# Kernel tuning notes

Measured on AMD Instinct MI355X. Metric: run time of the kernel, lower is better.

Reference implementation:

```python
import jax, jax.numpy as jnp
import numpy as np
import math

B = 2048
INPUT_SIZE = 1024
OUTPUT_SIZE = 512
SPONGE = 1024
ACT = 256
REC = 256
STORE = ACT + REC  # 512
DEPTH = 8
BDEPTH = 10
NEUTRAL_C = 1.0
SQRT2 = math.sqrt(2.0)


def _make_structure():
    # Deterministic stand-in for the module's random.sample-based recall wiring.
    rng = np.random.RandomState(0)
    half = (SPONGE + 1) // 2
    shuffle_perm = np.array([i // 2 + (i % 2) * half for i in range(SPONGE)], dtype=np.int64)
    unused = []
    recall = []
    for i in range(DEPTH):
        unused.extend(range(i * STORE, (i + 1) * STORE))
        sel = rng.choice(len(unused), size=REC, replace=False)
        sel_set = set(sel.tolist())
        recall.append([unused[k] for k in sorted(sel_set)])
        unused = [u for k, u in enumerate(unused) if k not in sel_set]
    out_mem = np.array(sorted(unused), dtype=np.int64)  # 2048 leftover memory columns
    bf_size = len(out_mem) + SPONGE  # 3072
    bf_depth = int(math.ceil(math.log2(bf_size)))  # 12
    bf_half = (bf_size + 1) // 2
    bf_perm = np.array([i // 2 + (i % 2) * bf_half for i in range(bf_size)], dtype=np.int64)
    return shuffle_perm, np.array(recall, dtype=np.int64), out_mem, bf_perm, bf_size, bf_depth


def setup_inputs() -> dict:
    key = jax.random.key(0)
    ks = jax.random.split(key, 6)
    shuffle_perm, recall_idx, out_mem_idx, bf_perm, bf_size, bf_depth = _make_structure()
    return {
        "X": jax.random.normal(ks[0], (B, INPUT_SIZE), jnp.float32),
        "scales": jnp.ones((INPUT_SIZE,), jnp.float32),
        "angles": jax.random.uniform(ks[1], (DEPTH, BDEPTH, SPONGE // 2), jnp.float32) * (2 * math.pi),
        "act_bias": jax.random.normal(ks[2], (DEPTH, ACT), jnp.float32),
        "act_activation": jax.random.normal(ks[3], (DEPTH, ACT), jnp.float32),
        "act_curvature": jax.random.normal(ks[4], (DEPTH, ACT), jnp.float32),
        "bf_angles": jax.random.uniform(ks[5], (bf_depth, bf_size // 2), jnp.float32) * (2 * math.pi),
        "shuffle_perm": jnp.asarray(shuffle_perm),
        "recall_idx": jnp.asarray(recall_idx),
        "output_mem_idx": jnp.asarray(out_mem_idx),
        "bf_perm": jnp.asarray(bf_perm),
    }


def _base_activation(x, c):
    # In the source, `a` is overwritten with torch.tensor(1.0), so a == 1.
    t = (math.pi / 4) / c
    y0 = (1.0 / c) * (1.0 / SQRT2 - math.cos(math.pi / 2))  # = 1/(c*sqrt(2))
    m0 = math.sin(math.pi / 2)  # = 1
    y1 = (1.0 / c) * (1.0 / SQRT2 - 1.0)
    m1 = math.sin(0.0)  # = 0
    mid = (1.0 / c) * (1.0 / SQRT2 - jnp.cos(math.pi / 4 + c * x))
    return jnp.where(x > t, y0 + m0 * (x - t), jnp.where(x < -t, y1 + m1 * (x + t), mid))


def _butterfly(x, angles, perm):
    # angles: [n_layers, exch]; shuffle -> Givens rotation per pair, extra passthrough
    exch = angles.shape[1]
    for j in range(angles.shape[0]):
        s = x[:, perm]
        x1, x2 = s[:, :exch], s[:, exch:2 * exch]
        ca, sa = jnp.cos(angles[j]), jnp.sin(angles[j])
        x = jnp.concatenate([ca * x1 + sa * x2, -sa * x1 + ca * x2, s[:, 2 * exch:]], axis=1)
    return x


def reference(X, scales, angles, act_bias, act_activation, act_curvature, bf_angles,
              shuffle_perm, recall_idx, output_mem_idx, bf_perm):
    Xs = X * scales
    sponge = Xs[:, :SPONGE]  # input_size == sponge_size: no zero pad, memory[0] is empty
    mem = jnp.zeros((Xs.shape[0], DEPTH * STORE), Xs.dtype)
    for i in range(DEPTH):
        sponge = _butterfly(sponge, angles[i], shuffle_perm)
        x1 = sponge[:, STORE:STORE + ACT] + act_bias[i]  # activation_position == store_size
        c = 0.5 * NEUTRAL_C * (act_curvature[i] + jnp.sqrt(act_curvature[i] ** 2 + 1.0))
        ap = _base_activation(x1, c)
        am = _base_activation(-x1, c)
        act_out = jnp.stack([ap, am], axis=2).reshape(ap.shape[0], 2 * ACT)  # interleave +/-
        mem = mem.at[:, i * STORE:(i + 1) * STORE].set(sponge[:, :STORE])
        recall = mem[:, recall_idx[i]]  # indices only address already-filled columns
        # [act_out | sponge[store:act_pos] (empty) | sponge[act_pos+ACT:] | recall]
        sponge = jnp.concatenate([act_out, sponge[:, STORE + ACT:], recall], axis=1)
    pre = jnp.concatenate([mem[:, output_mem_idx], sponge], axis=1)  # [B, 3072]
    out = _butterfly(pre, bf_angles, bf_perm)
    return out[:, :OUTPUT_SIZE]
```

## Files before the change

### kernel.cpp

```cpp
#include <hip/hip_runtime.h>
#include <math.h>

#define NB 2048
#define DEPTH 8

#define FTAB_OFF    0
#define BF01_OFF    81920
#define BFF_OFF     88064
#define ACT4_OFF    98304
#define PHYSA_OFF   106496
#define PHYSR_OFF   110592
#define PHYSO2_OFF  112640

#define MB0 4608
#define EXB 4608

#define WFENCE() asm volatile("s_waitcnt lgkmcnt(0)" ::: "memory")

__global__ void setup_kernel(const float* __restrict__ angles,
                             const float* __restrict__ bf_angles,
                             const float* __restrict__ act_bias,
                             const float* __restrict__ act_curv,
                             const int* __restrict__ recall_idx,
                             const int* __restrict__ out_mem_idx,
                             float* __restrict__ ws) {
    __shared__ int physL[4096];
    if (blockIdx.x < 200) {
        int id = blockIdx.x * 256 + threadIdx.x;
        if (id < 40960) {
            int w = id & 3, t = (id >> 2) & 255, dg = id >> 10;
            int d = dg / 5, g = dg - 5 * d;
            int a = 2 * (t & 127) + (t >> 7);
            int pair = (w == 0) ? a : (w == 1) ? (a + 256)
                     : (w == 2) ? (2 * a) : (2 * a + 1);
            int st = 2 * g + (w >> 1);
            float ang = angles[(d * 10 + st) * 512 + pair];
            float s, c; __sincosf(ang, &s, &c);
            ws[FTAB_OFF + 2 * id]     = c;
            ws[FTAB_OFF + 2 * id + 1] = s;
        } else if (id < 44032) {
            int e = id - 40960;
            int w = e & 3; int ti = e >> 2;
            int t = ti / 3; int i = ti - 3 * t;
            int a = t + 256 * i;
            int pair = (w == 0) ? a : (w == 1) ? (a + 768)
                     : (w == 2) ? (2 * a) : (2 * a + 1);
            int stage = (w < 2) ? 0 : 1;
            float ang = bf_angles[stage * 1536 + pair];
            float s, c; __sincosf(ang, &s, &c);
            ws[BF01_OFF + 2 * e]     = c;
            ws[BF01_OFF + 2 * e + 1] = s;
        } else if (id < 49152) {
            int e = id - 44032;
            int f = e >> 10; int rem = e & 1023; int t = rem >> 2; int w = rem & 3;
            int P;
            if (f == 0) P = 3 * t;
            else if (f < 4) { int k = 8 - 2 * f;
                              P = ((t >> (2 * f)) * (768 >> k)) + (t & ((256 >> k) - 1)); }
            else P = t;
            int pair = (w == 0) ? P : (w == 1) ? (P + 768)
                     : (w == 2) ? (2 * P) : (2 * P + 1);
            int stage = (w < 2) ? (2 + 2 * f) : (3 + 2 * f);
            float ang = bf_angles[stage * 1536 + pair];
            float s, c; __sincosf(ang, &s, &c);
            ws[BFF_OFF + 2 * e]     = c;
            ws[BFF_OFF + 2 * e + 1] = s;
        } else if (id < 51200) {
            int ida = id - 49152;
            float cu = act_curv[ida];
            float c  = 0.5f * (cu + sqrtf(cu * cu + 1.0f));
            ((float4*)(ws + ACT4_OFF))[ida] =
                make_float4(act_bias[ida], c, 1.0f / c, 0.0f);
        }
    } else {
        int tid = threadIdx.x;
        for (int e = tid; e < 4096; e += 256) {
            int v = e, p;
            for (;;) {
                int d = v >> 9, j = v & 511;
                if (d == 0)  { p = j; break; }
                if (j < 256) { p = 256 + d * 256 + j; break; }
                v = recall_idx[(d - 1) * 256 + (j - 256)];
            }
            physL[e] = p;
        }
        __syncthreads();
        int* pa = (int*)(ws + PHYSA_OFF);
        for (int e = tid; e < 2048; e += 256) {
            int d = e >> 8, t = e & 255;
            int a = 2 * (t & 127) + (t >> 7);
            pa[2 * e]     = 2 * physL[d * 512 + 2 * a];
            pa[2 * e + 1] = 2 * physL[d * 512 + 2 * a + 1];
        }
        int* pr = (int*)(ws + PHYSR_OFF);
        for (int e = tid; e < 2048; e += 256)
            pr[e] = 2 * physL[recall_idx[e]];
        int* po = (int*)(ws + PHYSO2_OFF);
        for (int e = tid; e < 3072; e += 256) {
            int tt = e / 12; int r = e - 12 * tt; int i = r >> 2; int k = r & 3;
            int a = tt + 256 * i;
            int tl2 = a >> 1, th2 = a & 1;
            int pos = tl2 + 1536 * th2 + 384 * k;
            po[e] = (pos < 2048) ? 2 * physL[out_mem_idx[pos]]
                                 : MB0 + 2 * (pos - 2048);
        }
    }
}

__device__ __forceinline__ float actf(float x, float c, float ic) {
    const float is2 = 0.70710678118654752f;
    float tt = 0.78539816339744831f * ic;
    float y0 = is2 * ic;
    float y1 = (is2 - 1.0f) * ic;
    float mid = ic * (is2 - __cosf(0.78539816339744831f + c * x));
    return x > tt ? (y0 + (x - tt)) : (x < -tt ? y1 : mid);
}

__launch_bounds__(64, 2)
__global__ void sponge_kernel(const float* __restrict__ X,
                              const float* __restrict__ scales,
                              const float* __restrict__ ws,
                              float* __restrict__ out) {
    __shared__ float L[6656];
    const int lane = threadIdx.x;
    const int rowA = blockIdx.x * 2;

    const float4* ftab   = (const float4*)(ws + FTAB_OFF);
    const float4* bf01   = (const float4*)(ws + BF01_OFF);
    const float4* bff    = (const float4*)(ws + BFF_OFF);
    const float4* act4   = (const float4*)(ws + ACT4_OFF);
    const int2*   physA  = (const int2*)(ws + PHYSA_OFF);
    const int*    physr  = (const int*)(ws + PHYSR_OFF);
    const int*    physo2 = (const int*)(ws + PHYSO2_OFF);

    float hA[4][4], hB[4][4];
    {
        const float* Xr0 = X + (size_t)rowA * 1024;
        const float* Xr1 = Xr0 + 1024;
#pragma unroll
        for (int q = 0; q < 4; ++q) {
            int tq = lane + 64 * q;
            int b  = (tq & 127) + (tq >> 7) * 512;
#pragma unroll
            for (int k = 0; k < 4; ++k) {
                float s = scales[b + 128 * k];
                hA[q][k] = Xr0[b + 128 * k] * s;
                hB[q][k] = Xr1[b + 128 * k] * s;
            }
        }
    }

#define DQUAD(cA, cB, i0, i1, i2, i3, F0, F1, F2, F3)                    \
    { float g0 =  (cA).x * (i0) + (cA).y * (i2);                         \
      float g2 = -(cA).y * (i0) + (cA).x * (i2);                         \
      float g1 =  (cA).z * (i1) + (cA).w * (i3);                         \
      float g3 = -(cA).w * (i1) + (cA).z * (i3);                         \
      F0 =  (cB).x * g0 + (cB).y * g1;                                   \
      F2 = -(cB).y * g0 + (cB).x * g1;                                   \
      F1 =  (cB).z * g2 + (cB).w * g3;                                   \
      F3 = -(cB).w * g2 + (cB).z * g3; }

    float4 cs[4][2];
    int fb = 0;
#define LOADC()                                                          \
    { _Pragma("unroll")                                                  \
      for (int q = 0; q < 4; ++q) {                                      \
          int tq = lane + 64 * q;                                        \
          cs[q][0] = ftab[fb + 2 * tq];                                  \
          cs[q][1] = ftab[fb + 2 * tq + 1];                              \
      } fb += 512; }

    LOADC();

#pragma unroll 1
    for (int d = 0; d < DEPTH; ++d) {
        float4 av[2][4]; int pr2[2][2]; int2 pmv[4];
#pragma unroll
        for (int q = 0; q < 2; ++q) {
            int k0 = (lane + 64 * q) >> 1;
#pragma unroll
            for (int j = 0; j < 4; ++j) av[q][j] = act4[d * 256 + k0 + 64 * j];
            int u = lane + 64 * q;
            pr2[q][0] = physr[d * 256 + u];
            pr2[q][1] = physr[d * 256 + u + 128];
        }
#pragma unroll
        for (int q = 0; q < 4; ++q) pmv[q] = physA[d * 256 + lane + 64 * q];

        for (int g = 0; g < 4; ++g) {
#pragma unroll
            for (int q = 0; q < 4; ++q) {
                int tq = lane + 64 * q;
                int tl = tq & 127, th = tq >> 7;
                int WI = 2 * (2 * (tl & 15) + 32 * th + 64 * (tl >> 4));
                float fA0, fA1, fA2, fA3, fB0, fB1, fB2, fB3;
                DQUAD(cs[q][0], cs[q][1], hA[q][0], hA[q][1], hA[q][2], hA[q][3],
                      fA0, fA1, fA2, fA3);
                DQUAD(cs[q][0], cs[q][1], hB[q][0], hB[q][1], hB[q][2], hB[q][3],
                      fB0, fB1, fB2, fB3);
                *(float4*)(L + EXB + WI)        = make_float4(fA0, fB0, fA1, fB1);
                *(float4*)(L + EXB + WI + 1024) = make_float4(fA2, fB2, fA3, fB3);
            }
            WFENCE();
            LOADC();
#pragma unroll
            for (int q = 0; q < 4; ++q) {
                int tq = lane + 64 * q;
                int tl = tq & 127, th = tq >> 7;
                int RI = 2 * ((tl & 1) + 2 * ((tl >> 2) & 15) + 32 * ((tl >> 1) & 1)
                             + 64 * (tl >> 6) + 512 * th);
                float2 e0 = *(const float2*)(L + EXB + RI);
                float2 e1 = *(const float2*)(L + EXB + RI + 256);
                float2 e2 = *(const float2*)(L + EXB + RI + 512);
                float2 e3 = *(const float2*)(L + EXB + RI + 768);
                hA[q][0] = e0.x; hB[q][0] = e0.y; hA[q][1] = e1.x; hB[q][1] = e1.y;
                hA[q][2] = e2.x; hB[q][2] = e2.y; hA[q][3] = e3.x; hB[q][3] = e3.y;
            }
            WFENCE();
        }

#pragma unroll
        for (int q = 0; q < 4; ++q) {
            int tq = lane + 64 * q;
            int tl = tq & 127, th = tq >> 7;
            int aq = 2 * tl + th;
            float fA0, fA1, fA2, fA3, fB0, fB1, fB2, fB3;
            DQUAD(cs[q][0], cs[q][1], hA[q][0], hA[q][1], hA[q][2], hA[q][3],
                  fA0, fA1, fA2, fA3);
            DQUAD(cs[q][0], cs[q][1], hB[q][0], hB[q][1], hB[q][2], hB[q][3],
                  fB0, fB1, fB2, fB3);
            *(float2*)(L + pmv[q].x) = make_float2(fA0, fB0);
            *(float2*)(L + pmv[q].y) = make_float2(fA1, fB1);
            *(float4*)(L + EXB + 4 * aq) = make_float4(fA2, fB2, fA3, fB3);
        }
        WFENCE();
        if (d < DEPTH - 1) LOADC();
        {
            const float* Z = L + EXB;
#pragma unroll
            for (int q = 0; q < 2; ++q) {
                int tq = lane + 64 * q;
                int k0 = tq >> 1;
                float sgn = (tq & 1) ? -1.0f : 1.0f;
                float2 z0 = *(const float2*)(Z + 2 * k0);
                float2 z1 = *(const float2*)(Z + 2 * k0 + 128);
                float2 z2 = *(const float2*)(Z + 2 * k0 + 256);
                float2 z3 = *(const float2*)(Z + 2 * k0 + 384);
                hA[q][0] = actf(sgn * (z0.x + av[q][0].x), av[q][0].y, av[q][0].z);
                hB[q][0] = actf(sgn * (z0.y + av[q][0].x), av[q][0].y, av[q][0].z);
                hA[q][1] = actf(sgn * (z1.x + av[q][1].x), av[q][1].y, av[q][1].z);
                hB[q][1] = actf(sgn * (z1.y + av[q][1].x), av[q][1].y, av[q][1].z);
                hA[q][2] = actf(sgn * (z2.x + av[q][2].x), av[q][2].y, av[q][2].z);
                hB[q][2] = actf(sgn * (z2.y + av[q][2].x), av[q][2].y, av[q][2].z);
                hA[q][3] = actf(sgn * (z3.x + av[q][3].x), av[q][3].y, av[q][3].z);
                hB[q][3] = actf(sgn * (z3.y + av[q][3].x), av[q][3].y, av[q][3].z);
            }
#pragma unroll
            for (int q = 0; q < 2; ++q) {
                int u = lane + 64 * q;
                float2 k0v = *(const float2*)(Z + 512 + 2 * u);
                float2 k1v = *(const float2*)(Z + 768 + 2 * u);
                float2 rc0 = *(const float2*)(L + pr2[q][0]);
                float2 rc1 = *(const float2*)(L + pr2[q][1]);
                hA[2 + q][0] = k0v.x; hB[2 + q][0] = k0v.y;
                hA[2 + q][1] = k1v.x; hB[2 + q][1] = k1v.y;
                hA[2 + q][2] = rc0.x; hB[2 + q][2] = rc0.y;
                hA[2 + q][3] = rc1.x; hB[2 + q][3] = rc1.y;
            }
        }
        WFENCE();
    }

    int4 pga[4][3];
#pragma unroll
    for (int q = 0; q < 4; ++q) {
        const int4* pgp = (const int4*)(physo2 + (lane + 64 * q) * 12);
#pragma unroll
        for (int j = 0; j < 3; ++j) pga[q][j] = pgp[j];
    }
#pragma unroll
    for (int q = 0; q < 4; ++q) {
        int tq = lane + 64 * q;
        int b  = (tq & 127) + (tq >> 7) * 512;
        *(float2*)(L + EXB + 2 * b)       = make_float2(hA[q][0], hB[q][0]);
        *(float2*)(L + EXB + 2 * b + 256) = make_float2(hA[q][1], hB[q][1]);
        *(float2*)(L + EXB + 2 * b + 512) = make_float2(hA[q][2], hB[q][2]);
        *(float2*)(L + EXB + 2 * b + 768) = make_float2(hA[q][3], hB[q][3]);
    }
    WFENCE();

    float2 w[4][12];
#pragma unroll
    for (int q = 0; q < 4; ++q) {
        int4 pg = pga[q][0];
        w[q][0] = *(const float2*)(L + pg.x); w[q][1] = *(const float2*)(L + pg.y);
        w[q][2] = *(const float2*)(L + pg.z); w[q][3] = *(const float2*)(L + pg.w);
        pg = pga[q][1];
        w[q][4] = *(const float2*)(L + pg.x); w[q][5] = *(const float2*)(L + pg.y);
        w[q][6] = *(const float2*)(L + pg.z); w[q][7] = *(const float2*)(L + pg.w);
        pg = pga[q][2];
        w[q][8]  = *(const float2*)(L + pg.x); w[q][9]  = *(const float2*)(L + pg.y);
        w[q][10] = *(const float2*)(L + pg.z); w[q][11] = *(const float2*)(L + pg.w);
    }
    WFENCE();

#pragma unroll
    for (int q = 0; q < 4; ++q) {
        int tq = lane + 64 * q;
#pragma unroll
        for (int i = 0; i < 3; ++i) {
            float4 c01 = bf01[(tq * 3 + i) * 2];
            float4 c23 = bf01[(tq * 3 + i) * 2 + 1];
            float yA0, yA1, yA2, yA3, yB0, yB1, yB2, yB3;
            DQUAD(c01, c23, w[q][4*i].x, w[q][4*i+1].x, w[q][4*i+2].x, w[q][4*i+3].x,
                  yA0, yA1, yA2, yA3);
            DQUAD(c01, c23, w[q][4*i].y, w[q][4*i+1].y, w[q][4*i+2].y, w[q][4*i+3].y,
                  yB0, yB1, yB2, yB3);
            *(float4*)(L + 4 * tq + 1024 * i)        = make_float4(yA0, yB0, yA1, yB1);
            *(float4*)(L + 4 * tq + 1024 * i + 3072) = make_float4(yA2, yB2, yA3, yB3);
        }
    }
    WFENCE();

#pragma unroll
    for (int f = 0; f < 4; ++f) {
        float2 x1p[4], x1r[4], x2p[4], x2r[4];
        float4 cS[4], cT[4];
        int Pq[4];
#pragma unroll
        for (int q = 0; q < 4; ++q) {
            int tq = lane + 64 * q;
            cS[q] = bff[(f * 256 + tq) * 2];
            cT[q] = bff[(f * 256 + tq) * 2 + 1];
            int P;
            if (f == 0) P = 3 * tq;
            else { const int k = 8 - 2 * f;
                   P = ((tq >> (2 * f)) * (768 >> k)) + (tq & ((256 >> k) - 1)); }
            Pq[q] = P;
            int base = 2 * ((P >> 1) + (P & 1) * 1536);
            x1p[q] = *(const float2*)(L + base);
            x1r[q] = *(const float2*)(L + base + 768);
            x2p[q] = *(const float2*)(L + base + 1536);
            x2r[q] = *(const float2*)(L + base + 2304);
        }
        WFENCE();
#pragma unroll
        for (int q = 0; q < 4; ++q) {
            float4 csS = cS[q], csT = cT[q];
            float o1P =  csS.x * x1p[q].x + csS.y * x2p[q].x;
            float o2P = -csS.y * x1p[q].x + csS.x * x2p[q].x;
            float o1Q =  csS.z * x1r[q].x + csS.w * x2r[q].x;
            float o2Q = -csS.w * x1r[q].x + csS.z * x2r[q].x;
            float yA0 =  csT.x * o1P + csT.y * o1Q;
            float yA2 = -csT.y * o1P + csT.x * o1Q;
            float yA1 =  csT.z * o2P + csT.w * o2Q;
            float yA3 = -csT.w * o2P + csT.z * o2Q;
            o1P =  csS.x * x1p[q].y + csS.y * x2p[q].y;
            o2P = -csS.y * x1p[q].y + csS.x * x2p[q].y;
            o1Q =  csS.z * x1r[q].y + csS.w * x2r[q].y;
            o2Q = -csS.w * x1r[q].y + csS.z * x2r[q].y;
            float yB0 =  csT.x * o1P + csT.y * o1Q;
            float yB2 = -csT.y * o1P + csT.x * o1Q;
            float yB1 =  csT.z * o2P + csT.w * o2Q;
            float yB3 = -csT.w * o2P + csT.z * o2Q;
            *(float4*)(L + 4 * Pq[q])        = make_float4(yA0, yB0, yA1, yB1);
            *(float4*)(L + 4 * Pq[q] + 3072) = make_float4(yA2, yB2, yA3, yB3);
        }
        WFENCE();
    }

#pragma unroll
    for (int q = 0; q < 4; ++q) {
        int tq = lane + 64 * q;
        int base = 2 * ((tq >> 1) + (tq & 1) * 1536);
        float4 csS = bff[(4 * 256 + tq) * 2];
        float4 csT = bff[(4 * 256 + tq) * 2 + 1];
        float2 x1p = *(const float2*)(L + base);
        float2 x1r = *(const float2*)(L + base + 768);
        float2 x2p = *(const float2*)(L + base + 1536);
        float2 x2r = *(const float2*)(L + base + 2304);
        float o1P =  csS.x * x1p.x + csS.y * x2p.x;
        float o2P = -csS.y * x1p.x + csS.x * x2p.x;
        float o1Q =  csS.z * x1r.x + csS.w * x2r.x;
        float o2Q = -csS.w * x1r.x + csS.z * x2r.x;
        *(float2*)(out + (size_t)rowA * 512 + 2 * tq) =
            make_float2(csT.x * o1P + csT.y * o1Q, csT.z * o2P + csT.w * o2Q);
        o1P =  csS.x * x1p.y + csS.y * x2p.y;
        o2P = -csS.y * x1p.y + csS.x * x2p.y;
        o1Q =  csS.z * x1r.y + csS.w * x2r.y;
        o2Q = -csS.w * x1r.y + csS.z * x2r.y;
        *(float2*)(out + (size_t)(rowA + 1) * 512 + 2 * tq) =
            make_float2(csT.x * o1P + csT.y * o1Q, csT.z * o2P + csT.w * o2Q);
    }
#undef DQUAD
#undef LOADC
}

extern "C" void kernel_launch(void* const* d_in, const int* in_sizes, int n_in,
                              void* d_out, int out_size, void* d_ws, size_t ws_size,
                              hipStream_t stream) {
    const float* X          = (const float*)d_in[0];
    const float* scales     = (const float*)d_in[1];
    const float* angles     = (const float*)d_in[2];
    const float* act_bias   = (const float*)d_in[3];
    const float* act_curv   = (const float*)d_in[5];
    const float* bf_angles  = (const float*)d_in[6];
    const int*   recall_idx  = (const int*)d_in[8];
    const int*   out_mem_idx = (const int*)d_in[9];

    float* ws = (float*)d_ws;

    setup_kernel<<<201, 256, 0, stream>>>(angles, bf_angles, act_bias, act_curv,
                                          recall_idx, out_mem_idx, ws);
    sponge_kernel<<<NB / 2, 64, 0, stream>>>(X, scales, ws, (float*)d_out);
}
```

Before: 134.1 us.

## Process one row per wave with four waves per block instead of two rows per wave

Each block now runs four 64-lane waves, and each wave handles a single row in its own LDS slice, where before one wave handled two interleaved rows. This halves the register state per lane and allows higher occupancy, trading away the shared reuse of twiddle coefficients across two rows. The explicit lgkmcnt fences are removed and relied on wave-local ordering instead. The setup kernel now resolves the recall chain level by level in LDS rather than by pointer-chasing through global memory.

Measured after the change: 123.1 us. 8.2% less time.

```diff
diff --git a/kernel.cpp b/kernel.cpp
--- a/kernel.cpp
+++ b/kernel.cpp
@@ -12,10 +12,8 @@
 #define PHYSR_OFF   110592
 #define PHYSO2_OFF  112640
 
-#define MB0 4608
-#define EXB 4608
-
-#define WFENCE() asm volatile("s_waitcnt lgkmcnt(0)" ::: "memory")
+#define EXB 2304
+#define RSZ 3328
 
 __global__ void setup_kernel(const float* __restrict__ angles,
                              const float* __restrict__ bf_angles,
@@ -25,6 +23,8 @@
                              const int* __restrict__ out_mem_idx,
                              float* __restrict__ ws) {
     __shared__ int physL[4096];
+    __shared__ int rcl[2048];
+    __shared__ int oml[2048];
     if (blockIdx.x < 200) {
         int id = blockIdx.x * 256 + threadIdx.x;
         if (id < 40960) {
@@ -74,35 +74,37 @@
         }
     } else {
         int tid = threadIdx.x;
-        for (int e = tid; e < 4096; e += 256) {
-            int v = e, p;
-            for (;;) {
-                int d = v >> 9, j = v & 511;
-                if (d == 0)  { p = j; break; }
-                if (j < 256) { p = 256 + d * 256 + j; break; }
-                v = recall_idx[(d - 1) * 256 + (j - 256)];
-            }
-            physL[e] = p;
-        }
+        for (int e = tid; e < 2048; e += 256) rcl[e] = recall_idx[e];
+        for (int e = tid; e < 2048; e += 256) oml[e] = out_mem_idx[e];
+        for (int e = tid; e < 512; e += 256) physL[e] = e;
         __syncthreads();
+        for (int d = 1; d < 8; ++d) {
+            for (int j = tid; j < 512; j += 256) {
+                int p;
+                if (j < 256) p = 256 + d * 256 + j;
+                else          p = physL[rcl[(d - 1) * 256 + (j - 256)]];
+                physL[512 * d + j] = p;
+            }
+            __syncthreads();
+        }
         int* pa = (int*)(ws + PHYSA_OFF);
         for (int e = tid; e < 2048; e += 256) {
             int d = e >> 8, t = e & 255;
             int a = 2 * (t & 127) + (t >> 7);
-            pa[2 * e]     = 2 * physL[d * 512 + 2 * a];
-            pa[2 * e + 1] = 2 * physL[d * 512 + 2 * a + 1];
+            pa[2 * e]     = physL[d * 512 + 2 * a];
+            pa[2 * e + 1] = physL[d * 512 + 2 * a + 1];
         }
         int* pr = (int*)(ws + PHYSR_OFF);
         for (int e = tid; e < 2048; e += 256)
-            pr[e] = 2 * physL[recall_idx[e]];
+            pr[e] = physL[rcl[e]];
         int* po = (int*)(ws + PHYSO2_OFF);
         for (int e = tid; e < 3072; e += 256) {
             int tt = e / 12; int r = e - 12 * tt; int i = r >> 2; int k = r & 3;
             int a = tt + 256 * i;
             int tl2 = a >> 1, th2 = a & 1;
             int pos = tl2 + 1536 * th2 + 384 * k;
-            po[e] = (pos < 2048) ? 2 * physL[out_mem_idx[pos]]
-                                 : MB0 + 2 * (pos - 2048);
+            po[e] = (pos < 2048) ? physL[oml[pos]]
+                                 : EXB + (pos - 2048);
         }
     }
 }
@@ -116,38 +118,44 @@
     return x > tt ? (y0 + (x - tt)) : (x < -tt ? y1 : mid);
 }
 
-__launch_bounds__(64, 2)
+__launch_bounds__(256, 3)
 __global__ void sponge_kernel(const float* __restrict__ X,
                               const float* __restrict__ scales,
                               const float* __restrict__ ws,
                               float* __restrict__ out) {
-    __shared__ float L[6656];
-    const int lane = threadIdx.x;
-    const int rowA = blockIdx.x * 2;
-
-    const float4* ftab   = (const float4*)(ws + FTAB_OFF);
-    const float4* bf01   = (const float4*)(ws + BF01_OFF);
-    const float4* bff    = (const float4*)(ws + BFF_OFF);
-    const float4* act4   = (const float4*)(ws + ACT4_OFF);
-    const int2*   physA  = (const int2*)(ws + PHYSA_OFF);
-    const int*    physr  = (const int*)(ws + PHYSR_OFF);
-    const int*    physo2 = (const int*)(ws + PHYSO2_OFF);
-
-    float hA[4][4], hB[4][4];
+    __shared__ float Lall[4 * RSZ];
+    const int lane = threadIdx.x & 63;
+    const int wvid = threadIdx.x >> 6;
+    float* __restrict__ L = Lall + wvid * RSZ;
+    const int row = blockIdx.x * 4 + wvid;
+
+    const float4* bf01  = (const float4*)(ws + BF01_OFF);
+    const float4* bff   = (const float4*)(ws + BFF_OFF);
+    const float4* act4  = (const float4*)(ws + ACT4_OFF);
+    const int2* physA  = (const int2*)(ws + PHYSA_OFF);
+    const int*  physr  = (const int*)(ws + PHYSR_OFF);
+    const int*  physo2 = (const int*)(ws + PHYSO2_OFF);
+
+    int Wn[4], Rn[4], Bq[4], Aq[4];
+#pragma unroll
+    for (int q = 0; q < 4; ++q) {
+        int tq = lane + 64 * q;
+        int tl = tq & 127, th = tq >> 7;
+        Wn[q] = 2 * (tl & 15) + 32 * th + 64 * (tl >> 4);
+        Rn[q] = (tl & 1) + 2 * ((tl >> 2) & 15) + 32 * ((tl >> 1) & 1)
+              + 64 * (tl >> 6) + 512 * th;
+        Bq[q] = tl + th * 512;
+        Aq[q] = 2 * tl + th;
+    }
+
+    float h[4][4];
     {
-        const float* Xr0 = X + (size_t)rowA * 1024;
-        const float* Xr1 = Xr0 + 1024;
-#pragma unroll
-        for (int q = 0; q < 4; ++q) {
-            int tq = lane + 64 * q;
-            int b  = (tq & 127) + (tq >> 7) * 512;
-#pragma unroll
-            for (int k = 0; k < 4; ++k) {
-                float s = scales[b + 128 * k];
-                hA[q][k] = Xr0[b + 128 * k] * s;
-                hB[q][k] = Xr1[b + 128 * k] * s;
-            }
-        }
+        const float* Xr = X + (size_t)row * 1024;
+#pragma unroll
+        for (int q = 0; q < 4; ++q)
+#pragma unroll
+            for (int k = 0; k < 4; ++k)
+                h[q][k] = Xr[Bq[q] + 128 * k] * scales[Bq[q] + 128 * k];
     }
 
 #define DQUAD(cA, cB, i0, i1, i2, i3, F0, F1, F2, F3)                    \
@@ -158,18 +166,18 @@
       F0 =  (cB).x * g0 + (cB).y * g1;                                   \
       F2 = -(cB).y * g0 + (cB).x * g1;                                   \
       F1 =  (cB).z * g2 + (cB).w * g3;                                   \
-      F3 = -(cB).w * g2 + (cB).z * g3; }
-
-    float4 cs[4][2];
+      F3 =  -(cB).w * g2 + (cB).z * g3; }
+
+    const float4* ftab = (const float4*)(ws + FTAB_OFF);
     int fb = 0;
+    float4 csA[4], csB[4];
 #define LOADC()                                                          \
     { _Pragma("unroll")                                                  \
       for (int q = 0; q < 4; ++q) {                                      \
           int tq = lane + 64 * q;                                        \
-          cs[q][0] = ftab[fb + 2 * tq];                                  \
-          cs[q][1] = ftab[fb + 2 * tq + 1];                              \
+          csA[q] = ftab[fb + 2 * tq];                                    \
+          csB[q] = ftab[fb + 2 * tq + 1];                                \
       } fb += 512; }
-
     LOADC();
 
 #pragma unroll 1
@@ -177,98 +185,70 @@
         float4 av[2][4]; int pr2[2][2]; int2 pmv[4];
 #pragma unroll
         for (int q = 0; q < 2; ++q) {
-            int k0 = (lane + 64 * q) >> 1;
+            int tq = lane + 64 * q;
+            int k0 = tq >> 1;
 #pragma unroll
             for (int j = 0; j < 4; ++j) av[q][j] = act4[d * 256 + k0 + 64 * j];
-            int u = lane + 64 * q;
-            pr2[q][0] = physr[d * 256 + u];
-            pr2[q][1] = physr[d * 256 + u + 128];
+            pr2[q][0] = physr[d * 256 + tq];
+            pr2[q][1] = physr[d * 256 + tq + 128];
         }
 #pragma unroll
         for (int q = 0; q < 4; ++q) pmv[q] = physA[d * 256 + lane + 64 * q];
 
+#pragma unroll
         for (int g = 0; g < 4; ++g) {
+            float f[4][4];
+#pragma unroll
+            for (int q = 0; q < 4; ++q)
+                DQUAD(csA[q], csB[q], h[q][0], h[q][1], h[q][2], h[q][3],
+                      f[q][0], f[q][1], f[q][2], f[q][3]);
 #pragma unroll
             for (int q = 0; q < 4; ++q) {
-                int tq = lane + 64 * q;
-                int tl = tq & 127, th = tq >> 7;
-                int WI = 2 * (2 * (tl & 15) + 32 * th + 64 * (tl >> 4));
-                float fA0, fA1, fA2, fA3, fB0, fB1, fB2, fB3;
-                DQUAD(cs[q][0], cs[q][1], hA[q][0], hA[q][1], hA[q][2], hA[q][3],
-                      fA0, fA1, fA2, fA3);
-                DQUAD(cs[q][0], cs[q][1], hB[q][0], hB[q][1], hB[q][2], hB[q][3],
-                      fB0, fB1, fB2, fB3);
-                *(float4*)(L + EXB + WI)        = make_float4(fA0, fB0, fA1, fB1);
-                *(float4*)(L + EXB + WI + 1024) = make_float4(fA2, fB2, fA3, fB3);
-            }
-            WFENCE();
+                *(float2*)(L + EXB + Wn[q])       = make_float2(f[q][0], f[q][1]);
+                *(float2*)(L + EXB + Wn[q] + 512) = make_float2(f[q][2], f[q][3]);
+            }
             LOADC();
 #pragma unroll
             for (int q = 0; q < 4; ++q) {
-                int tq = lane + 64 * q;
-                int tl = tq & 127, th = tq >> 7;
-                int RI = 2 * ((tl & 1) + 2 * ((tl >> 2) & 15) + 32 * ((tl >> 1) & 1)
-                             + 64 * (tl >> 6) + 512 * th);
-                float2 e0 = *(const float2*)(L + EXB + RI);
-                float2 e1 = *(const float2*)(L + EXB + RI + 256);
-                float2 e2 = *(const float2*)(L + EXB + RI + 512);
-                float2 e3 = *(const float2*)(L + EXB + RI + 768);
-                hA[q][0] = e0.x; hB[q][0] = e0.y; hA[q][1] = e1.x; hB[q][1] = e1.y;
-                hA[q][2] = e2.x; hB[q][2] = e2.y; hA[q][3] = e3.x; hB[q][3] = e3.y;
-            }
-            WFENCE();
-        }
-
-#pragma unroll
-        for (int q = 0; q < 4; ++q) {
-            int tq = lane + 64 * q;
-            int tl = tq & 127, th = tq >> 7;
-            int aq = 2 * tl + th;
-            float fA0, fA1, fA2, fA3, fB0, fB1, fB2, fB3;
-            DQUAD(cs[q][0], cs[q][1], hA[q][0], hA[q][1], hA[q][2], hA[q][3],
-                  fA0, fA1, fA2, fA3);
-            DQUAD(cs[q][0], cs[q][1], hB[q][0], hB[q][1], hB[q][2], hB[q][3],
-                  fB0, fB1, fB2, fB3);
-            *(float2*)(L + pmv[q].x) = make_float2(fA0, fB0);
-            *(float2*)(L + pmv[q].y) = make_float2(fA1, fB1);
-            *(float4*)(L + EXB + 4 * aq) = make_float4(fA2, fB2, fA3, fB3);
-        }
-        WFENCE();
-        if (d < DEPTH - 1) LOADC();
+                h[q][0] = L[EXB + Rn[q]];
+                h[q][1] = L[EXB + Rn[q] + 128];
+                h[q][2] = L[EXB + Rn[q] + 256];
+                h[q][3] = L[EXB + Rn[q] + 384];
+            }
+        }
         {
+            float f[4][4];
+#pragma unroll
+            for (int q = 0; q < 4; ++q)
+                DQUAD(csA[q], csB[q], h[q][0], h[q][1], h[q][2], h[q][3],
+                      f[q][0], f[q][1], f[q][2], f[q][3]);
+#pragma unroll
+            for (int q = 0; q < 4; ++q) {
+                L[pmv[q].x] = f[q][0];
+                L[pmv[q].y] = f[q][1];
+                *(float2*)(L + EXB + 2 * Aq[q]) = make_float2(f[q][2], f[q][3]);
+            }
+            if (d < DEPTH - 1) LOADC();
             const float* Z = L + EXB;
 #pragma unroll
             for (int q = 0; q < 2; ++q) {
                 int tq = lane + 64 * q;
                 int k0 = tq >> 1;
                 float sgn = (tq & 1) ? -1.0f : 1.0f;
-                float2 z0 = *(const float2*)(Z + 2 * k0);
-                float2 z1 = *(const float2*)(Z + 2 * k0 + 128);
-                float2 z2 = *(const float2*)(Z + 2 * k0 + 256);
-                float2 z3 = *(const float2*)(Z + 2 * k0 + 384);
-                hA[q][0] = actf(sgn * (z0.x + av[q][0].x), av[q][0].y, av[q][0].z);
-                hB[q][0] = actf(sgn * (z0.y + av[q][0].x), av[q][0].y, av[q][0].z);
-                hA[q][1] = actf(sgn * (z1.x + av[q][1].x), av[q][1].y, av[q][1].z);
-                hB[q][1] = actf(sgn * (z1.y + av[q][1].x), av[q][1].y, av[q][1].z);
-                hA[q][2] = actf(sgn * (z2.x + av[q][2].x), av[q][2].y, av[q][2].z);
-                hB[q][2] = actf(sgn * (z2.y + av[q][2].x), av[q][2].y, av[q][2].z);
-                hA[q][3] = actf(sgn * (z3.x + av[q][3].x), av[q][3].y, av[q][3].z);
-                hB[q][3] = actf(sgn * (z3.y + av[q][3].x), av[q][3].y, av[q][3].z);
+                h[q][0] = actf(sgn * (Z[k0]       + av[q][0].x), av[q][0].y, av[q][0].z);
+                h[q][1] = actf(sgn * (Z[k0 + 64]  + av[q][1].x), av[q][1].y, av[q][1].z);
+                h[q][2] = actf(sgn * (Z[k0 + 128] + av[q][2].x), av[q][2].y, av[q][2].z);
+                h[q][3] = actf(sgn * (Z[k0 + 192] + av[q][3].x), av[q][3].y, av[q][3].z);
             }
 #pragma unroll
             for (int q = 0; q < 2; ++q) {
                 int u = lane + 64 * q;
-                float2 k0v = *(const float2*)(Z + 512 + 2 * u);
-                float2 k1v = *(const float2*)(Z + 768 + 2 * u);
-                float2 rc0 = *(const float2*)(L + pr2[q][0]);
-                float2 rc1 = *(const float2*)(L + pr2[q][1]);
-                hA[2 + q][0] = k0v.x; hB[2 + q][0] = k0v.y;
-                hA[2 + q][1] = k1v.x; hB[2 + q][1] = k1v.y;
-                hA[2 + q][2] = rc0.x; hB[2 + q][2] = rc0.y;
-                hA[2 + q][3] = rc1.x; hB[2 + q][3] = rc1.y;
-            }
-        }
-        WFENCE();
+                h[2 + q][0] = Z[256 + u];
+                h[2 + q][1] = Z[384 + u];
+                h[2 + q][2] = L[pr2[q][0]];
+                h[2 + q][3] = L[pr2[q][1]];
+            }
+        }
     }
 
     int4 pga[4][3];
@@ -280,30 +260,21 @@
     }
 #pragma unroll
     for (int q = 0; q < 4; ++q) {
-        int tq = lane + 64 * q;
-        int b  = (tq & 127) + (tq >> 7) * 512;
-        *(float2*)(L + EXB + 2 * b)       = make_float2(hA[q][0], hB[q][0]);
-        *(float2*)(L + EXB + 2 * b + 256) = make_float2(hA[q][1], hB[q][1]);
-        *(float2*)(L + EXB + 2 * b + 512) = make_float2(hA[q][2], hB[q][2]);
-        *(float2*)(L + EXB + 2 * b + 768) = make_float2(hA[q][3], hB[q][3]);
-    }
-    WFENCE();
-
-    float2 w[4][12];
+        L[EXB + Bq[q]]       = h[q][0];
+        L[EXB + Bq[q] + 128] = h[q][1];
+        L[EXB + Bq[q] + 256] = h[q][2];
+        L[EXB + Bq[q] + 384] = h[q][3];
+    }
+    float w[4][12];
 #pragma unroll
     for (int q = 0; q < 4; ++q) {
         int4 pg = pga[q][0];
-        w[q][0] = *(const float2*)(L + pg.x); w[q][1] = *(const float2*)(L + pg.y);
-        w[q][2] = *(const float2*)(L + pg.z); w[q][3] = *(const float2*)(L + pg.w);
+        w[q][0] = L[pg.x]; w[q][1] = L[pg.y]; w[q][2] = L[pg.z]; w[q][3] = L[pg.w];
         pg = pga[q][1];
-        w[q][4] = *(const float2*)(L + pg.x); w[q][5] = *(const float2*)(L + pg.y);
-        w[q][6] = *(const float2*)(L + pg.z); w[q][7] = *(const float2*)(L + pg.w);
+        w[q][4] = L[pg.x]; w[q][5] = L[pg.y]; w[q][6] = L[pg.z]; w[q][7] = L[pg.w];
         pg = pga[q][2];
-        w[q][8]  = *(const float2*)(L + pg.x); w[q][9]  = *(const float2*)(L + pg.y);
-        w[q][10] = *(const float2*)(L + pg.z); w[q][11] = *(const float2*)(L + pg.w);
-    }
-    WFENCE();
-
+        w[q][8] = L[pg.x]; w[q][9] = L[pg.y]; w[q][10] = L[pg.z]; w[q][11] = L[pg.w];
+    }
 #pragma unroll
     for (int q = 0; q < 4; ++q) {
         int tq = lane + 64 * q;
@@ -311,86 +282,63 @@
         for (int i = 0; i < 3; ++i) {
             float4 c01 = bf01[(tq * 3 + i) * 2];
             float4 c23 = bf01[(tq * 3 + i) * 2 + 1];
-            float yA0, yA1, yA2, yA3, yB0, yB1, yB2, yB3;
-            DQUAD(c01, c23, w[q][4*i].x, w[q][4*i+1].x, w[q][4*i+2].x, w[q][4*i+3].x,
-                  yA0, yA1, yA2, yA3);
-            DQUAD(c01, c23, w[q][4*i].y, w[q][4*i+1].y, w[q][4*i+2].y, w[q][4*i+3].y,
-                  yB0, yB1, yB2, yB3);
-            *(float4*)(L + 4 * tq + 1024 * i)        = make_float4(yA0, yB0, yA1, yB1);
-            *(float4*)(L + 4 * tq + 1024 * i + 3072) = make_float4(yA2, yB2, yA3, yB3);
-        }
-    }
-    WFENCE();
-
+            float y0, y1, y2, y3;
+            DQUAD(c01, c23, w[q][4 * i], w[q][4 * i + 1], w[q][4 * i + 2], w[q][4 * i + 3],
+                  y0, y1, y2, y3);
+            *(float2*)(L + 2 * tq + 512 * i)        = make_float2(y0, y1);
+            *(float2*)(L + 2 * tq + 512 * i + 1536) = make_float2(y2, y3);
+        }
+    }
 #pragma unroll
     for (int f = 0; f < 4; ++f) {
-        float2 x1p[4], x1r[4], x2p[4], x2r[4];
-        float4 cS[4], cT[4];
-        int Pq[4];
+        float x1[4], x2[4], x3[4], x4[4];
+        float4 cS[4], cT[4]; int Pq[4];
 #pragma unroll
         for (int q = 0; q < 4; ++q) {
             int tq = lane + 64 * q;
-            cS[q] = bff[(f * 256 + tq) * 2];
-            cT[q] = bff[(f * 256 + tq) * 2 + 1];
             int P;
             if (f == 0) P = 3 * tq;
             else { const int k = 8 - 2 * f;
                    P = ((tq >> (2 * f)) * (768 >> k)) + (tq & ((256 >> k) - 1)); }
             Pq[q] = P;
-            int base = 2 * ((P >> 1) + (P & 1) * 1536);
-            x1p[q] = *(const float2*)(L + base);
-            x1r[q] = *(const float2*)(L + base + 768);
-            x2p[q] = *(const float2*)(L + base + 1536);
-            x2r[q] = *(const float2*)(L + base + 2304);
-        }
-        WFENCE();
+            int base = (P >> 1) + (P & 1) * 1536;
+            cS[q] = bff[(f * 256 + tq) * 2];
+            cT[q] = bff[(f * 256 + tq) * 2 + 1];
+            x1[q] = L[base];
+            x2[q] = L[base + 384];
+            x3[q] = L[base + 768];
+            x4[q] = L[base + 1152];
+        }
 #pragma unroll
         for (int q = 0; q < 4; ++q) {
-            float4 csS = cS[q], csT = cT[q];
-            float o1P =  csS.x * x1p[q].x + csS.y * x2p[q].x;
-            float o2P = -csS.y * x1p[q].x + csS.x * x2p[q].x;
-            float o1Q =  csS.z * x1r[q].x + csS.w * x2r[q].x;
-            float o2Q = -csS.w * x1r[q].x + csS.z * x2r[q].x;
-            float yA0 =  csT.x * o1P + csT.y * o1Q;
-            float yA2 = -csT.y * o1P + csT.x * o1Q;
-            float yA1 =  csT.z * o2P + csT.w * o2Q;
-            float yA3 = -csT.w * o2P + csT.z * o2Q;
-            o1P =  csS.x * x1p[q].y + csS.y * x2p[q].y;
-            o2P = -csS.y * x1p[q].y + csS.x * x2p[q].y;
-            o1Q =  csS.z * x1r[q].y + csS.w * x2r[q].y;
-            o2Q = -csS.w * x1r[q].y + csS.z * x2r[q].y;
-            float yB0 =  csT.x * o1P + csT.y * o1Q;
-            float yB2 = -csT.y * o1P + csT.x * o1Q;
-            float yB1 =  csT.z * o2P + csT.w * o2Q;
-            float yB3 = -csT.w * o2P + csT.z * o2Q;
-            *(float4*)(L + 4 * Pq[q])        = make_float4(yA0, yB0, yA1, yB1);
-            *(float4*)(L + 4 * Pq[q] + 3072) = make_float4(yA2, yB2, yA3, yB3);
-        }
-        WFENCE();
-    }
-
+            float o1P =  cS[q].x * x1[q] + cS[q].y * x3[q];
+            float o2P = -cS[q].y * x1[q] + cS[q].x * x3[q];
+            float o1Q =  cS[q].z * x2[q] + cS[q].w * x4[q];
+            float o2Q = -cS[q].w * x2[q] + cS[q].z * x4[q];
+            float y0 =  cT[q].x * o1P + cT[q].y * o1Q;
+            float y2 = -cT[q].y * o1P + cT[q].x * o1Q;
+            float y1 =  cT[q].z * o2P + cT[q].w * o2Q;
+            float y3 = -cT[q].w * o2P + cT[q].z * o2Q;
+            *(float2*)(L + 2 * Pq[q])        = make_float2(y0, y1);
+            *(float2*)(L + 2 * Pq[q] + 1536) = make_float2(y2, y3);
+        }
+    }
 #pragma unroll
     for (int q = 0; q < 4; ++q) {
         int tq = lane + 64 * q;
-        int base = 2 * ((tq >> 1) + (tq & 1) * 1536);
-        float4 csS = bff[(4 * 256 + tq) * 2];
-        float4 csT = bff[(4 * 256 + tq) * 2 + 1];
-        float2 x1p = *(const float2*)(L + base);
-        float2 x1r = *(const float2*)(L + base + 768);
-        float2 x2p = *(const float2*)(L + base + 1536);
-        float2 x2r = *(const float2*)(L + base + 2304);
-        float o1P =  csS.x * x1p.x + csS.y * x2p.x;
-        float o2P = -csS.y * x1p.x + csS.x * x2p.x;
-        float o1Q =  csS.z * x1r.x + csS.w * x2r.x;
-        float o2Q = -csS.w * x1r.x + csS.z * x2r.x;
-        *(float2*)(out + (size_t)rowA * 512 + 2 * tq) =
-            make_float2(csT.x * o1P + csT.y * o1Q, csT.z * o2P + csT.w * o2Q);
-        o1P =  csS.x * x1p.y + csS.y * x2p.y;
-        o2P = -csS.y * x1p.y + csS.x * x2p.y;
-        o1Q =  csS.z * x1r.y + csS.w * x2r.y;
-        o2Q = -csS.w * x1r.y + csS.z * x2r.y;
-        *(float2*)(out + (size_t)(rowA + 1) * 512 + 2 * tq) =
-            make_float2(csT.x * o1P + csT.y * o1Q, csT.z * o2P + csT.w * o2Q);
+        int base = (tq >> 1) + (tq & 1) * 1536;
+        float4 cS = bff[(4 * 256 + tq) * 2];
+        float4 cT = bff[(4 * 256 + tq) * 2 + 1];
+        float x1 = L[base];
+        float x2 = L[base + 384];
+        float x3 = L[base + 768];
+        float x4 = L[base + 1152];
+        float o1P =  cS.x * x1 + cS.y * x3;
+        float o2P = -cS.y * x1 + cS.x * x3;
+        float o1Q =  cS.z * x2 + cS.w * x4;
+        float o2Q = -cS.w * x2 + cS.z * x4;
+        *(float2*)(out + (size_t)row * 512 + 2 * tq) =
+            make_float2(cT.x * o1P + cT.y * o1Q, cT.z * o2P + cT.w * o2Q);
     }
 #undef DQUAD
 #undef LOADC
@@ -412,5 +360,5 @@
 
     setup_kernel<<<201, 256, 0, stream>>>(angles, bf_angles, act_bias, act_curv,
                                           recall_idx, out_mem_idx, ws);
-    sponge_kernel<<<NB / 2, 64, 0, stream>>>(X, scales, ws, (float*)d_out);
+    sponge_kernel<<<NB / 4, 256, 0, stream>>>(X, scales, ws, (float*)d_out);
 }
```
